# Performance work log

Hardware: AMD Instinct MI355X
Metric: run time of the kernel (lower is better)

The kernel has to match this reference:

```python
import jax, jax.numpy as jnp
import numpy as np

NSAMPLE = 32
LAMBDA = 0.5


def setup_inputs() -> dict:
    key = jax.random.key(0)
    k1, k2, k3, k4, k5 = jax.random.split(key, 5)
    B, N, NPOINT, C, NCOMP = 4, 8192, 2048, 64, 16
    xyz = jax.random.normal(k1, (B, N, 3), dtype=jnp.float32)
    new_xyz = jax.random.normal(k2, (B, NPOINT, 3), dtype=jnp.float32)
    components = jax.random.randint(k3, (B, N, 1), 0, NCOMP, dtype=jnp.int64)
    new_components = jax.random.randint(k4, (B, NPOINT, 1), 0, NCOMP, dtype=jnp.int64)
    features = jax.random.normal(k5, (B, C, N), dtype=jnp.float32)
    return {"xyz": xyz, "new_xyz": new_xyz, "components": components,
            "new_components": new_components, "features": features}


def _gag_knn(new_xyz, xyz, new_comp, comp, k, lam):
    # squared pairwise distances (B, npoint, N), same math as sum((src-dst)**2)
    diff = new_xyz[:, :, None, :] - xyz[:, None, :, :]
    dists = jnp.sum(diff * diff, axis=-1)
    # component-aware rescale
    mask = comp[:, None, :] == new_comp[:, :, None]  # (B, npoint, N)
    dists = jnp.where(mask, dists * lam, dists * (1.0 - lam))
    # full argsort then take first k (faithful to original)
    idx = jnp.argsort(dists, axis=-1)[:, :, :k]  # (B, npoint, k)
    return idx.astype(jnp.int32)


def reference(xyz, new_xyz, components, new_components, features):
    comp = components[..., 0]
    new_comp = new_components[..., 0]
    idx = _gag_knn(new_xyz, xyz, new_comp, comp, NSAMPLE, LAMBDA)  # (B, npoint, ns)

    # group xyz: gather along N -> (B, npoint, ns, 3)
    grouped_xyz = jnp.take_along_axis(xyz[:, None, :, :], idx[..., None], axis=2)
    grouped_xyz = grouped_xyz - new_xyz[:, :, None, :]
    grouped_xyz = jnp.transpose(grouped_xyz, (0, 3, 1, 2))  # (B, 3, npoint, ns)

    # group features: (B, C, N) -> (B, npoint, ns, C) -> (B, C, npoint, ns)
    feats_bnc = jnp.transpose(features, (0, 2, 1))  # (B, N, C)
    grouped_feats = jnp.take_along_axis(feats_bnc[:, None, :, :], idx[..., None], axis=2)
    grouped_feats = jnp.transpose(grouped_feats, (0, 3, 1, 2))  # (B, C, npoint, ns)

    return jnp.concatenate([grouped_xyz, grouped_feats], axis=1)  # (B, 3+C, npoint, ns)
```

## Files before the change

kernel.cpp:

```cpp
#include <hip/hip_runtime.h>


#define BQ 4
#define NN_ 8192
#define NPOINT 2048
#define CF 64
#define NS 32
#define T1 256
#define PER (NN_ / T1)
#define QB 8
#define CAPQ 128
#define M_EPS 1e-3f

#define KNN_BLOCKS (BQ * NPOINT / QB)
#define TR_BLOCKS  ((NN_ / 32) * (CF / 32) * BQ)

#define REG_A (QB * T1 * 4)
#define REG_B (QB * CAPQ * 4)
#define SMEM_BYTES (REG_A + REG_B + QB * 4 + QB * 4)

__device__ __forceinline__ float rfl(float x) {
  return __int_as_float(__builtin_amdgcn_readfirstlane(__float_as_int(x)));
}

__global__ __launch_bounds__(256) void knn_tr_kernel(
    const float* __restrict__ xyz, const float* __restrict__ new_xyz,
    const float* __restrict__ features, int* __restrict__ idxOut,
    float* __restrict__ featsT) {
  __shared__ __align__(16) char smem[SMEM_BYTES];
  const int tid = threadIdx.x;

  if (blockIdx.x >= KNN_BLOCKS) {
    float(*tr)[33] = (float(*)[33])smem;
    const int t = blockIdx.x - KNN_BLOCKS;
    const int n0 = (t & 255) * 32;
    const int c0 = ((t >> 8) & 1) * 32;
    const int b = t >> 9;
    const int tx = tid & 31;
    const int ty = tid >> 5;
#pragma unroll
    for (int i = 0; i < 4; i++) {
      int c = c0 + ty + i * 8;
      tr[ty + i * 8][tx] = features[(size_t)b * CF * NN_ + (size_t)c * NN_ + n0 + tx];
    }
    __syncthreads();
#pragma unroll
    for (int i = 0; i < 4; i++) {
      int nrow = n0 + ty + i * 8;
      featsT[(size_t)b * NN_ * CF + (size_t)nrow * CF + c0 + tx] = tr[tx][ty + i * 8];
    }
    return;
  }

  float(*sMin)[T1] = (float(*)[T1])smem;
  unsigned long long(*keys)[CAPQ] = (unsigned long long(*)[CAPQ])smem;
  unsigned int(*candI)[CAPQ] = (unsigned int(*)[CAPQ])(smem + REG_A);
  float* sTheta = (float*)(smem + REG_A + REG_B);
  int* cnt = (int*)(smem + REG_A + REG_B + QB * 4);

  const int tile = blockIdx.x;
  const int b = tile / (NPOINT / QB);
  const int q0 = b * NPOINT + (tile % (NPOINT / QB)) * QB;
  const int lane = tid & 63;
  const int wid = tid >> 6;

  float qx2[QB], qy2[QB], qz2[QB], qnn[QB];
#pragma unroll
  for (int k = 0; k < QB; k++) {
    float ax = new_xyz[(q0 + k) * 3 + 0];
    float ay = new_xyz[(q0 + k) * 3 + 1];
    float az = new_xyz[(q0 + k) * 3 + 2];
    qx2[k] = rfl(-2.0f * ax);
    qy2[k] = rfl(-2.0f * ay);
    qz2[k] = rfl(-2.0f * az);
    qnn[k] = rfl(ax * ax + ay * ay + az * az);
  }

  const float4* __restrict__ base4 = (const float4*)(xyz + (size_t)b * NN_ * 3);

  float smin_r[QB];
#pragma unroll
  for (int k = 0; k < QB; k++) smin_r[k] = 3.4e38f;

#pragma unroll 2
  for (int g = 0; g < PER / 4; g++) {
    const int v = g * 768 + tid * 3;
    float4 v0 = base4[v + 0];
    float4 v1 = base4[v + 1];
    float4 v2 = base4[v + 2];
    float xs[4] = {v0.x, v0.w, v1.z, v2.y};
    float ys[4] = {v0.y, v1.x, v1.w, v2.z};
    float zs[4] = {v0.z, v1.y, v2.x, v2.w};
#pragma unroll
    for (int i = 0; i < 4; i++) {
      float pp = fmaf(zs[i], zs[i], fmaf(ys[i], ys[i], xs[i] * xs[i]));
#pragma unroll
      for (int k = 0; k < QB; k++) {
        float t = fmaf(xs[i], qx2[k], pp);
        t = fmaf(ys[i], qy2[k], t);
        t = fmaf(zs[i], qz2[k], t);
        smin_r[k] = fminf(smin_r[k], t);
      }
    }
  }

#pragma unroll
  for (int k = 0; k < QB; k++) sMin[k][tid] = smin_r[k];
  if (tid < QB) cnt[tid] = 0;
  __syncthreads();

#pragma unroll
  for (int t2 = 0; t2 < 2; t2++) {
    const int k = wid * 2 + t2;
    float m = fminf(fminf(sMin[k][lane], sMin[k][lane + 64]),
                    fminf(sMin[k][lane + 128], sMin[k][lane + 192]));
#pragma unroll
    for (int kk = 2; kk <= 64; kk <<= 1) {
#pragma unroll
      for (int jj = kk >> 1; jj > 0; jj >>= 1) {
        float o = __shfl_xor(m, jj);
        bool up = ((lane & kk) == 0);
        bool lower = ((lane & jj) == 0);
        m = (up == lower) ? fminf(m, o) : fmaxf(m, o);
      }
    }
    if (lane == 31) sTheta[k] = m + qnn[k] + M_EPS;
  }
  __syncthreads();

  float th2[QB];
#pragma unroll
  for (int k = 0; k < QB; k++)
    th2[k] = rfl(sTheta[k] + M_EPS - qnn[k]);

#pragma unroll 1
  for (int g = 0; g < PER / 4; g++) {
    const int v = g * 768 + tid * 3;
    float4 v0 = base4[v + 0];
    float4 v1 = base4[v + 1];
    float4 v2 = base4[v + 2];
    float xs[4] = {v0.x, v0.w, v1.z, v2.y};
    float ys[4] = {v0.y, v1.x, v1.w, v2.z};
    float zs[4] = {v0.z, v1.y, v2.x, v2.w};
#pragma unroll
    for (int i = 0; i < 4; i++) {
      float pp = fmaf(zs[i], zs[i], fmaf(ys[i], ys[i], xs[i] * xs[i]));
      const int n = g * 1024 + tid * 4 + i;
#pragma unroll
      for (int k = 0; k < QB; k++) {
        float t = fmaf(xs[i], qx2[k], pp);
        t = fmaf(ys[i], qy2[k], t);
        t = fmaf(zs[i], qz2[k], t);
        if (t <= th2[k]) {
          int pos = atomicAdd(&cnt[k], 1);
          if (pos < CAPQ) candI[k][pos] = (unsigned)n;
        }
      }
    }
  }
  __syncthreads();

  const float* __restrict__ baseF = xyz + (size_t)b * NN_ * 3;
#pragma unroll
  for (int t2 = 0; t2 < 2; t2++) {
    const int k = wid * 2 + t2;
    const int qq = q0 + k;
    const int m = cnt[k] < CAPQ ? cnt[k] : CAPQ;
    const float qxk = new_xyz[qq * 3 + 0];
    const float qyk = new_xyz[qq * 3 + 1];
    const float qzk = new_xyz[qq * 3 + 2];

    unsigned long long keyreg[CAPQ / 64];
#pragma unroll
    for (int c = 0; c < CAPQ / 64; c++) {
      const int i = lane + c * 64;
      if (i < m) {
        const int n = (int)candI[k][i];
        float dx = baseF[n * 3 + 0] - qxk;
        float dy = baseF[n * 3 + 1] - qyk;
        float dz = baseF[n * 3 + 2] - qzk;
        float d = __fadd_rn(__fadd_rn(__fmul_rn(dx, dx), __fmul_rn(dy, dy)),
                            __fmul_rn(dz, dz));
        keyreg[c] = ((unsigned long long)__float_as_uint(d) << 32) | (unsigned)n;
      }
    }
    __syncthreads();
#pragma unroll
    for (int c = 0; c < CAPQ / 64; c++) {
      const int i = lane + c * 64;
      if (i < m) keys[k][i] = keyreg[c];
    }
    __syncthreads();
#pragma unroll
    for (int c = 0; c < CAPQ / 64; c++) {
      const int i = lane + c * 64;
      if (i < m) {
        unsigned long long x = keys[k][i];
        int r = 0;
        for (int j = 0; j < m; j++) r += (keys[k][j] < x) ? 1 : 0;
        if (r < NS) idxOut[qq * NS + r] = (int)(x & 0xffffffffu);
      }
    }
    __syncthreads();
  }
}

#define FSTR 68
__global__ __launch_bounds__(256) void group_kernel(const float* __restrict__ xyz,
                                                    const float* __restrict__ new_xyz,
                                                    const float* __restrict__ featsT,
                                                    const int* __restrict__ idxArr,
                                                    float* __restrict__ out) {
  const int q = blockIdx.x;
  const int b = q / NPOINT;
  const int p = q - b * NPOINT;
  const int tid = threadIdx.x;

  __shared__ int sIdx[NS];
  __shared__ __align__(16) float ldsF[NS * FSTR];
  __shared__ float ldsX[3 * NS];

  if (tid < NS) sIdx[tid] = idxArr[q * NS + tid];
  __syncthreads();

  {
    int s = tid >> 3, r = tid & 7;
    int nn = sIdx[s];
    const float4* src = (const float4*)(featsT + ((size_t)b * NN_ + nn) * CF);
    float4 v0 = src[r * 2];
    float4 v1 = src[r * 2 + 1];
    float4* dst = (float4*)(ldsF + s * FSTR + r * 8);
    dst[0] = v0;
    dst[1] = v1;
  }
  if (tid < 96) {
    int dd = tid >> 5, s = tid & 31;
    int nn = sIdx[s];
    ldsX[dd * NS + s] = xyz[((size_t)b * NN_ + nn) * 3 + dd] -
                        new_xyz[(size_t)q * 3 + dd];
  }
  __syncthreads();

  const int s = tid & 31;
  const int r0 = tid >> 5;
#pragma unroll
  for (int k = 0; k < 9; k++) {
    int row = r0 + k * 8;
    if (row < 67) {
      float v = (row < 3) ? ldsX[row * NS + s] : ldsF[s * FSTR + (row - 3)];
      out[(((size_t)b * 67 + row) * NPOINT + p) * NS + s] = v;
    }
  }
}

extern "C" void kernel_launch(void* const* d_in, const int* in_sizes, int n_in,
                              void* d_out, int out_size, void* d_ws, size_t ws_size,
                              hipStream_t stream) {
  const float* xyz      = (const float*)d_in[0];
  const float* new_xyz  = (const float*)d_in[1];
  const float* features = (const float*)d_in[4];
  float* out = (float*)d_out;

  int* idxArr = (int*)d_ws;
  float* featsT = (float*)((char*)d_ws + (size_t)BQ * NPOINT * NS * sizeof(int));

  knn_tr_kernel<<<KNN_BLOCKS + TR_BLOCKS, T1, 0, stream>>>(xyz, new_xyz, features,
                                                           idxArr, featsT);
  group_kernel<<<BQ * NPOINT, T1, 0, stream>>>(xyz, new_xyz, featsT, idxArr, out);
}
```

Baseline: 129.3 us.

## Fuse KNN and grouping into one kernel, gather features directly from channel-major layout

Merges the KNN kernel and the grouping kernel into one launch. Each block keeps its selected neighbor indices in LDS and writes the grouped xyz and features straight to the output. The separate feature transpose pass and the global index and transposed-feature workspace round trips are dropped. Features are now gathered as scattered scalar loads from the (B,C,N) layout. These are less coalesced than the float4 row loads from the transposed copy, and the output writes run at the KNN grid size of only 1024 blocks.

```diff
diff --git a/kernel.cpp b/kernel.cpp
--- a/kernel.cpp
+++ b/kernel.cpp
@@ -13,54 +13,32 @@
 #define M_EPS 1e-3f
 
 #define KNN_BLOCKS (BQ * NPOINT / QB)
-#define TR_BLOCKS  ((NN_ / 32) * (CF / 32) * BQ)
 
 #define REG_A (QB * T1 * 4)
 #define REG_B (QB * CAPQ * 4)
-#define SMEM_BYTES (REG_A + REG_B + QB * 4 + QB * 4)
+#define SMEM_BYTES (REG_A + REG_B)
 
 __device__ __forceinline__ float rfl(float x) {
   return __int_as_float(__builtin_amdgcn_readfirstlane(__float_as_int(x)));
 }
 
-__global__ __launch_bounds__(256) void knn_tr_kernel(
+__global__ __launch_bounds__(256) void fused_kernel(
     const float* __restrict__ xyz, const float* __restrict__ new_xyz,
-    const float* __restrict__ features, int* __restrict__ idxOut,
-    float* __restrict__ featsT) {
+    const float* __restrict__ features, float* __restrict__ out) {
   __shared__ __align__(16) char smem[SMEM_BYTES];
-  const int tid = threadIdx.x;
-
-  if (blockIdx.x >= KNN_BLOCKS) {
-    float(*tr)[33] = (float(*)[33])smem;
-    const int t = blockIdx.x - KNN_BLOCKS;
-    const int n0 = (t & 255) * 32;
-    const int c0 = ((t >> 8) & 1) * 32;
-    const int b = t >> 9;
-    const int tx = tid & 31;
-    const int ty = tid >> 5;
-#pragma unroll
-    for (int i = 0; i < 4; i++) {
-      int c = c0 + ty + i * 8;
-      tr[ty + i * 8][tx] = features[(size_t)b * CF * NN_ + (size_t)c * NN_ + n0 + tx];
-    }
-    __syncthreads();
-#pragma unroll
-    for (int i = 0; i < 4; i++) {
-      int nrow = n0 + ty + i * 8;
-      featsT[(size_t)b * NN_ * CF + (size_t)nrow * CF + c0 + tx] = tr[tx][ty + i * 8];
-    }
-    return;
-  }
+  __shared__ float sTheta[QB];
+  __shared__ int cnt[QB];
+  __shared__ int sIdxLds[QB][NS];
 
   float(*sMin)[T1] = (float(*)[T1])smem;
   unsigned long long(*keys)[CAPQ] = (unsigned long long(*)[CAPQ])smem;
   unsigned int(*candI)[CAPQ] = (unsigned int(*)[CAPQ])(smem + REG_A);
-  float* sTheta = (float*)(smem + REG_A + REG_B);
-  int* cnt = (int*)(smem + REG_A + REG_B + QB * 4);
-
+
+  const int tid = threadIdx.x;
   const int tile = blockIdx.x;
   const int b = tile / (NPOINT / QB);
-  const int q0 = b * NPOINT + (tile % (NPOINT / QB)) * QB;
+  const int p0 = (tile % (NPOINT / QB)) * QB;
+  const int q0 = b * NPOINT + p0;
   const int lane = tid & 63;
   const int wid = tid >> 6;
 
@@ -198,58 +176,40 @@
         unsigned long long x = keys[k][i];
         int r = 0;
         for (int j = 0; j < m; j++) r += (keys[k][j] < x) ? 1 : 0;
-        if (r < NS) idxOut[qq * NS + r] = (int)(x & 0xffffffffu);
+        if (r < NS) sIdxLds[k][r] = (int)(x & 0xffffffffu);
       }
     }
     __syncthreads();
   }
-}
-
-#define FSTR 68
-__global__ __launch_bounds__(256) void group_kernel(const float* __restrict__ xyz,
-                                                    const float* __restrict__ new_xyz,
-                                                    const float* __restrict__ featsT,
-                                                    const int* __restrict__ idxArr,
-                                                    float* __restrict__ out) {
-  const int q = blockIdx.x;
-  const int b = q / NPOINT;
-  const int p = q - b * NPOINT;
-  const int tid = threadIdx.x;
-
-  __shared__ int sIdx[NS];
-  __shared__ __align__(16) float ldsF[NS * FSTR];
-  __shared__ float ldsX[3 * NS];
-
-  if (tid < NS) sIdx[tid] = idxArr[q * NS + tid];
-  __syncthreads();
-
-  {
-    int s = tid >> 3, r = tid & 7;
-    int nn = sIdx[s];
-    const float4* src = (const float4*)(featsT + ((size_t)b * NN_ + nn) * CF);
-    float4 v0 = src[r * 2];
-    float4 v1 = src[r * 2 + 1];
-    float4* dst = (float4*)(ldsF + s * FSTR + r * 8);
-    dst[0] = v0;
-    dst[1] = v1;
-  }
-  if (tid < 96) {
-    int dd = tid >> 5, s = tid & 31;
-    int nn = sIdx[s];
-    ldsX[dd * NS + s] = xyz[((size_t)b * NN_ + nn) * 3 + dd] -
-                        new_xyz[(size_t)q * 3 + dd];
-  }
-  __syncthreads();
-
-  const int s = tid & 31;
-  const int r0 = tid >> 5;
-#pragma unroll
-  for (int k = 0; k < 9; k++) {
-    int row = r0 + k * 8;
-    if (row < 67) {
-      float v = (row < 3) ? ldsX[row * NS + s] : ldsF[s * FSTR + (row - 3)];
-      out[(((size_t)b * 67 + row) * NPOINT + p) * NS + s] = v;
-    }
+
+  const float* __restrict__ featB = features + (size_t)b * CF * NN_;
+#pragma unroll 1
+  for (int it = 0; it < 16; it++) {
+    const int idx = it * 256 + tid;
+    const int k = idx >> 9;
+    const int c = (idx >> 3) & 63;
+    const int g = idx & 7;
+    const int n0 = sIdxLds[k][g * 4 + 0];
+    const int n1 = sIdxLds[k][g * 4 + 1];
+    const int n2 = sIdxLds[k][g * 4 + 2];
+    const int n3 = sIdxLds[k][g * 4 + 3];
+    const float* fr = featB + (size_t)c * NN_;
+    float4 v = {fr[n0], fr[n1], fr[n2], fr[n3]};
+    *(float4*)&out[(((size_t)b * 67 + (3 + c)) * NPOINT + (p0 + k)) * NS + g * 4] = v;
+  }
+  if (tid < 192) {
+    const int k = tid / 24;
+    const int rem = tid - k * 24;
+    const int r = rem >> 3;
+    const int g = rem & 7;
+    const float qr = new_xyz[(q0 + k) * 3 + r];
+    const int n0 = sIdxLds[k][g * 4 + 0];
+    const int n1 = sIdxLds[k][g * 4 + 1];
+    const int n2 = sIdxLds[k][g * 4 + 2];
+    const int n3 = sIdxLds[k][g * 4 + 3];
+    float4 v = {baseF[n0 * 3 + r] - qr, baseF[n1 * 3 + r] - qr,
+                baseF[n2 * 3 + r] - qr, baseF[n3 * 3 + r] - qr};
+    *(float4*)&out[(((size_t)b * 67 + r) * NPOINT + (p0 + k)) * NS + g * 4] = v;
   }
 }
 
@@ -261,10 +221,5 @@
   const float* features = (const float*)d_in[4];
   float* out = (float*)d_out;
 
-  int* idxArr = (int*)d_ws;
-  float* featsT = (float*)((char*)d_ws + (size_t)BQ * NPOINT * NS * sizeof(int));
-
-  knn_tr_kernel<<<KNN_BLOCKS + TR_BLOCKS, T1, 0, stream>>>(xyz, new_xyz, features,
-                                                           idxArr, featsT);
-  group_kernel<<<BQ * NPOINT, T1, 0, stream>>>(xyz, new_xyz, featsT, idxArr, out);
+  fused_kernel<<<KNN_BLOCKS, T1, 0, stream>>>(xyz, new_xyz, features, out);
 }
```

After: 182.5 us. +41.1%, slower.
